# Performance work log

Hardware: AMD Instinct MI355X
Metric: run time of the kernel (lower is better)

## Reference

```python
import jax, jax.numpy as jnp
import numpy as np

S, B, I, H = 512, 8192, 3, 5  # seq, batch, input_size, hidden_size


def _uniform(key, shape, bound):
    return jax.random.uniform(key, shape, jnp.float32, -bound, bound)


def setup_inputs() -> dict:
    key = jax.random.key(0)
    ks = jax.random.split(key, 17)
    bound = 1.0 / np.sqrt(H)
    inp = {"x": jax.random.normal(ks[0], (S, B, I), jnp.float32)}
    # layer 0: in=I ; layer 1: in=2H (concat of both directions). Suffix 'r' = reverse direction.
    specs = [
        ("l0", I), ("l0r", I), ("l1", 2 * H), ("l1r", 2 * H),
    ]
    ki = 1
    for name, din in specs:
        inp[f"w_ih_{name}"] = _uniform(ks[ki], (4 * H, din), bound); ki += 1
        inp[f"w_hh_{name}"] = _uniform(ks[ki], (4 * H, H), bound); ki += 1
        inp[f"b_ih_{name}"] = _uniform(ks[ki], (4 * H,), bound); ki += 1
        inp[f"b_hh_{name}"] = _uniform(ks[ki], (4 * H,), bound); ki += 1
    return inp


def _lstm_dir(x, w_ih, w_hh, b_ih, b_hh, reverse):
    """Single-direction LSTM over x [S,B,Din] -> (hs [S,B,H], h_T [B,H], c_T [B,H])."""
    xs = x[::-1] if reverse else x
    # Precompute input contributions for all timesteps in one big matmul.
    gx = jnp.einsum('sbi,gi->sbg', xs, w_ih) + b_ih + b_hh  # [S,B,4H]
    h0 = jnp.zeros((x.shape[1], H), x.dtype)
    c0 = jnp.zeros((x.shape[1], H), x.dtype)

    def step(carry, g):
        h, c = carry
        g = g + h @ w_hh.T  # [B,4H]
        i, f, gg, o = jnp.split(g, 4, axis=-1)  # PyTorch gate order: i,f,g,o
        i = jax.nn.sigmoid(i)
        f = jax.nn.sigmoid(f)
        gg = jnp.tanh(gg)
        o = jax.nn.sigmoid(o)
        c = f * c + i * gg
        h = o * jnp.tanh(c)
        return (h, c), h

    (hT, cT), hs = jax.lax.scan(step, (h0, c0), gx)
    if reverse:
        hs = hs[::-1]
    return hs, hT, cT


def reference(x,
              w_ih_l0, w_hh_l0, b_ih_l0, b_hh_l0,
              w_ih_l0r, w_hh_l0r, b_ih_l0r, b_hh_l0r,
              w_ih_l1, w_hh_l1, b_ih_l1, b_hh_l1,
              w_ih_l1r, w_hh_l1r, b_ih_l1r, b_hh_l1r):
    # Layer 0 (bidirectional)
    hs0f, h0f, c0f = _lstm_dir(x, w_ih_l0, w_hh_l0, b_ih_l0, b_hh_l0, False)
    hs0b, h0b, c0b = _lstm_dir(x, w_ih_l0r, w_hh_l0r, b_ih_l0r, b_hh_l0r, True)
    out0 = jnp.concatenate([hs0f, hs0b], axis=-1)  # [S,B,2H]
    # Layer 1 (bidirectional) consumes concat of both directions
    hs1f, h1f, c1f = _lstm_dir(out0, w_ih_l1, w_hh_l1, b_ih_l1, b_hh_l1, False)
    hs1b, h1b, c1b = _lstm_dir(out0, w_ih_l1r, w_hh_l1r, b_ih_l1r, b_hh_l1r, True)
    output = jnp.concatenate([hs1f, hs1b], axis=-1)  # [S,B,2H]
    # PyTorch h_n/c_n layout: [num_layers*num_directions, B, H] ordered (l0 fwd, l0 bwd, l1 fwd, l1 bwd)
    h_n = jnp.stack([h0f, h0b, h1f, h1b], axis=0)
    c_n = jnp.stack([c0f, c0b, c1f, c1b], axis=0)
    return output, h_n, c_n
```

## Files before the change

kernel.cpp:

```cpp
#include <hip/hip_runtime.h>


constexpr int S_ = 512;
constexpr int B_ = 8192;
constexpr int NROW = 16384;

constexpr int GD1  = 2048;
constexpr int TL   = 240;
constexpr int GSTR = GD1 * 64;

constexpr float L2E  = 1.4426950408889634f;
constexpr float T2E  = 2.8853900817779268f;
constexpr float IT2E = 0.34657359027997264f;

typedef _Float16 v2h __attribute__((ext_vector_type(2)));

__device__ __forceinline__ float dot2h(v2h a, v2h b, float c) {
#if __has_builtin(__builtin_amdgcn_fdot2)
    return __builtin_amdgcn_fdot2(a, b, c, false);
#else
    return fmaf((float)a[0], (float)b[0], fmaf((float)a[1], (float)b[1], c));
#endif
}

__device__ __forceinline__ float rcp_(float x) { return __builtin_amdgcn_rcpf(x); }

__device__ __forceinline__ float exp2_(float x) {
#if __has_builtin(__builtin_amdgcn_exp2f)
    return __builtin_amdgcn_exp2f(x);
#else
    return exp2f(x);
#endif
}

__device__ __forceinline__ void sbar() { __builtin_amdgcn_sched_barrier(0); }

__device__ __forceinline__ float bperm(int bidx, float v) {
    return __int_as_float(__builtin_amdgcn_ds_bpermute(bidx, __float_as_int(v)));
}

__device__ __forceinline__ unsigned pkh(float a, float b) {
    auto t = __builtin_amdgcn_cvt_pkrtz(a, b);
    unsigned q; __builtin_memcpy(&q, &t, 4); return q;
}

__device__ __forceinline__ unsigned short f2h(float x) {
    _Float16 h = (_Float16)x;
    unsigned short s; __builtin_memcpy(&s, &h, 2); return s;
}

__device__ __forceinline__ float h2f(unsigned short s) {
    _Float16 h; __builtin_memcpy(&h, &s, 2); return (float)h;
}

__global__ __launch_bounds__(64) __attribute__((amdgpu_waves_per_eu(1, 2)))
void lstm_layer0(
    const float* __restrict__ x,
    const float* __restrict__ wih_f, const float* __restrict__ whh_f,
    const float* __restrict__ bih_f, const float* __restrict__ bhh_f,
    const float* __restrict__ wih_r, const float* __restrict__ whh_r,
    const float* __restrict__ bih_r, const float* __restrict__ bhh_r,
    unsigned short* __restrict__ ws,
    float* __restrict__ outbase)
{
    const int l64 = threadIdx.x & 63;
    int r = l64 / 5; r = (r > 11) ? 11 : r;
    const int u   = l64 - r * 5;
    const int uc  = (u < 5) ? u : 4;
    const int gid = blockIdx.x * 12 + r;
    const bool valid = gid < NROW;
    const int dir = (gid >> 13) & 1;
    const int b   = gid & 8191;
    const bool stw = valid && (u < 3);
    const bool st  = valid && (u < 5);

    int bidx[5];
#pragma unroll
    for (int k = 0; k < 5; k++) bidx[k] = (r * 5 + k) * 4;

    const float* __restrict__ wih = dir ? wih_r : wih_f;
    const float* __restrict__ whh = dir ? whh_r : whh_f;
    const float* __restrict__ bih = dir ? bih_r : bih_f;
    const float* __restrict__ bhh = dir ? bhh_r : bhh_f;

    const int rows[4] = {uc, 5 + uc, 10 + uc, 15 + uc};
    const float scl[4] = {-L2E, -L2E, T2E, -L2E};
    float WX[4][3], WH[4][5], BS[4];
#pragma unroll
    for (int gi = 0; gi < 4; gi++) {
        const int rr = rows[gi]; const float sc = scl[gi];
#pragma unroll
        for (int i = 0; i < 3; i++) WX[gi][i] = wih[rr * 3 + i] * sc;
#pragma unroll
        for (int k = 0; k < 5; k++) WH[gi][k] = whh[rr * 5 + k] * sc;
        BS[gi] = (bih[rr] + bhh[rr]) * sc;
    }

    float h[5] = {0.f, 0.f, 0.f, 0.f, 0.f};
    float cp = 0.f, hu_last = 0.f;

    const int t0 = dir ? (S_ - 1) : 0;
    const float* xp = x + ((size_t)t0 * B_ + b) * 3;
    unsigned short* wp = ws + (size_t)dir * ((size_t)S_ * B_ * 6)
                            + ((size_t)t0 * B_ + b) * 6;
    const ptrdiff_t xst = dir ? -(ptrdiff_t)3 * B_ : (ptrdiff_t)3 * B_;
    const ptrdiff_t wst = dir ? -(ptrdiff_t)6 * B_ : (ptrdiff_t)6 * B_;

    auto step = [&](const float (&xin)[3], unsigned short* wpp) {
        float a0 = BS[0], a1 = BS[1], a2 = BS[2], a3 = BS[3];
#pragma unroll
        for (int i = 0; i < 3; i++) {
            a0 = fmaf(WX[0][i], xin[i], a0);
            a1 = fmaf(WX[1][i], xin[i], a1);
            a2 = fmaf(WX[2][i], xin[i], a2);
            a3 = fmaf(WX[3][i], xin[i], a3);
        }
#pragma unroll
        for (int k = 0; k < 5; k++) {
            a0 = fmaf(WH[0][k], h[k], a0);
            a1 = fmaf(WH[1][k], h[k], a1);
            a2 = fmaf(WH[2][k], h[k], a2);
            a3 = fmaf(WH[3][k], h[k], a3);
        }
        const float ig = rcp_(1.0f + exp2_(a0));
        const float fg = rcp_(1.0f + exp2_(a1));
        const float g2 = fmaf(-2.0f * T2E, rcp_(1.0f + exp2_(a2)), T2E);
        const float og = rcp_(1.0f + exp2_(a3));
        cp = fmaf(fg, cp, ig * g2);
        const float th = fmaf(-2.0f, rcp_(1.0f + exp2_(cp)), 1.0f);
        const float hu = og * th;
        hu_last = hu;
#pragma unroll
        for (int k = 0; k < 5; k++) h[k] = bperm(bidx[k], hu);
        const unsigned q0 = pkh(h[0], h[1]);
        const unsigned q1 = pkh(h[2], h[3]);
        const unsigned q2 = pkh(h[4], 0.0f);
        unsigned qs = q0;
        qs = (u == 1) ? q1 : qs;
        qs = (u == 2) ? q2 : qs;
        if (stw) ((unsigned*)wpp)[u] = qs;
    };

    auto ld = [&](float (&buf)[3]) {
        __builtin_memcpy(&buf[0], xp, 12);
        xp += xst;
        sbar();
    };

    float x0[3], x1[3], x2[3], x3[3], x4[3], x5[3], x6[3], x7[3];
    ld(x0); ld(x1); ld(x2); ld(x3); ld(x4); ld(x5); ld(x6); ld(x7);

#pragma unroll 1
    for (int s = 0; s < S_ - 8; s += 8) {
        step(x0, wp); wp += wst; ld(x0);
        step(x1, wp); wp += wst; ld(x1);
        step(x2, wp); wp += wst; ld(x2);
        step(x3, wp); wp += wst; ld(x3);
        step(x4, wp); wp += wst; ld(x4);
        step(x5, wp); wp += wst; ld(x5);
        step(x6, wp); wp += wst; ld(x6);
        step(x7, wp); wp += wst; ld(x7);
    }
    step(x0, wp); wp += wst;
    step(x1, wp); wp += wst;
    step(x2, wp); wp += wst;
    step(x3, wp); wp += wst;
    step(x4, wp); wp += wst;
    step(x5, wp); wp += wst;
    step(x6, wp); wp += wst;
    step(x7, wp);

    const size_t OUTE = (size_t)S_ * B_ * 10;
    float* hn = outbase + OUTE + ((size_t)dir * B_ + b) * 5;
    float* cn = hn + (size_t)4 * B_ * 5;
    if (st) { hn[uc] = hu_last; cn[uc] = cp * IT2E; }
}

__global__ __launch_bounds__(64) __attribute__((amdgpu_waves_per_eu(2, 4)))
void lstm_layer1(
    const unsigned short* __restrict__ ws,
    const float* __restrict__ wih_f, const float* __restrict__ whh_f,
    const float* __restrict__ bih_f, const float* __restrict__ bhh_f,
    const float* __restrict__ wih_r, const float* __restrict__ whh_r,
    const float* __restrict__ bih_r, const float* __restrict__ bhh_r,
    float* __restrict__ outbase,
    unsigned short* __restrict__ gtemp)
{
    __shared__ unsigned short lt[TL * 40];

    const int l64 = threadIdx.x & 63;
    const int bid = (int)blockIdx.x;
    const int bsw = (bid & 7) * 256 + (bid >> 3);
    const int r  = l64 >> 3;
    const int u  = l64 & 7;
    const int uc = (u < 5) ? u : 4;
    const int rm  = r & 3;
    const int dir = r >> 2;
    const int b   = bsw * 4 + rm;
    const bool st = (u < 5);
    const int dir5 = dir * 5;
    const int pr  = dir ? (r - 4) : (r + 4);
    const int psL = pr * 5 + uc;
    const int psG = pr * 8 + uc;

    const float* __restrict__ wih = dir ? wih_r : wih_f;
    const float* __restrict__ whh = dir ? whh_r : whh_f;
    const float* __restrict__ bih = dir ? bih_r : bih_f;
    const float* __restrict__ bhh = dir ? bhh_r : bhh_f;

    const int rows[4] = {uc, 5 + uc, 10 + uc, 15 + uc};
    const float scl[4] = {-L2E, -L2E, T2E, -L2E};
    v2h WX[4][6];
    float WH[4][5], BS[4];
#pragma unroll
    for (int gi = 0; gi < 4; gi++) {
        const int rr = rows[gi]; const float sc = scl[gi];
#pragma unroll
        for (int p = 0; p < 6; p++) {
            const int i0 = (p < 3) ? 2 * p : 2 * p - 1;
            const bool pad = (p == 2) || (p == 5);
            const float w0 = wih[rr * 10 + i0] * sc;
            const float w1 = pad ? 0.f : wih[rr * 10 + i0 + 1] * sc;
            WX[gi][p] = (v2h){(_Float16)w0, (_Float16)w1};
        }
#pragma unroll
        for (int k = 0; k < 5; k++) WH[gi][k] = whh[rr * 5 + k] * sc;
        BS[gi] = (bih[rr] + bhh[rr]) * sc;
    }

    float h[5] = {0.f, 0.f, 0.f, 0.f, 0.f};
    float cp = 0.f, hu_last = 0.f;

    const int t0 = dir ? (S_ - 1) : 0;
    const unsigned short* rpf = ws + ((size_t)t0 * B_ + b) * 6;
    const unsigned short* rpb = rpf + (size_t)S_ * B_ * 6;
    float* op = outbase + ((size_t)(dir ? 255 : 256) * B_ + b) * 10;
    const ptrdiff_t rst = dir ? -(ptrdiff_t)6 * B_ : (ptrdiff_t)6 * B_;
    const ptrdiff_t ost = dir ? -(ptrdiff_t)10 * B_ : (ptrdiff_t)10 * B_;

    unsigned short* gw = gtemp + (size_t)bid * 64 + l64;

    struct A4 { float a0, a1, a2, a3; };

    auto dots = [&](const v2h (&xin)[6]) -> A4 {
        A4 v;
        v.a0 = BS[0]; v.a1 = BS[1]; v.a2 = BS[2]; v.a3 = BS[3];
#pragma unroll
        for (int p = 0; p < 6; p++) {
            v.a0 = dot2h(xin[p], WX[0][p], v.a0);
            v.a1 = dot2h(xin[p], WX[1][p], v.a1);
            v.a2 = dot2h(xin[p], WX[2][p], v.a2);
            v.a3 = dot2h(xin[p], WX[3][p], v.a3);
        }
        return v;
    };

    auto cell = [&](A4 v) -> float {
#pragma unroll
        for (int k = 0; k < 5; k++) {
            v.a0 = fmaf(WH[0][k], h[k], v.a0);
            v.a1 = fmaf(WH[1][k], h[k], v.a1);
            v.a2 = fmaf(WH[2][k], h[k], v.a2);
            v.a3 = fmaf(WH[3][k], h[k], v.a3);
        }
        const float ig = rcp_(1.0f + exp2_(v.a0));
        const float fg = rcp_(1.0f + exp2_(v.a1));
        const float g2 = fmaf(-2.0f * T2E, rcp_(1.0f + exp2_(v.a2)), T2E);
        const float og = rcp_(1.0f + exp2_(v.a3));
        cp = fmaf(fg, cp, ig * g2);
        const float th = fmaf(-2.0f, rcp_(1.0f + exp2_(cp)), 1.0f);
        const float hu = og * th;
        hu_last = hu;
        return hu;
    };

    auto bcast = [&](float hu) {
        const int v = __float_as_int(hu);
        h[0] = __int_as_float(__builtin_amdgcn_ds_swizzle(v, 0x18 | (0 << 5)));
        h[1] = __int_as_float(__builtin_amdgcn_ds_swizzle(v, 0x18 | (1 << 5)));
        h[2] = __int_as_float(__builtin_amdgcn_ds_swizzle(v, 0x18 | (2 << 5)));
        h[3] = __int_as_float(__builtin_amdgcn_ds_swizzle(v, 0x18 | (3 << 5)));
        h[4] = __int_as_float(__builtin_amdgcn_ds_swizzle(v, 0x18 | (4 << 5)));
    };

    auto ld = [&](v2h (&buf)[6]) {
        __builtin_memcpy(&buf[0], rpf, 12);
        __builtin_memcpy(&buf[3], rpb, 12);
        rpf += rst; rpb += rst;
        sbar();
    };

    auto s1L = [&](v2h (&xb)[6], int t) {
        A4 a = dots(xb); ld(xb);
        const float hu = cell(a); bcast(hu);
        if (st) lt[t * 40 + r * 5 + u] = f2h(hu);
    };
    auto s1G = [&](v2h (&xb)[6]) {
        A4 a = dots(xb); ld(xb);
        const float hu = cell(a); bcast(hu);
        *gw = f2h(hu); gw += GSTR;
    };
    auto s2G = [&](v2h (&xb)[6], unsigned short pvs) {
        A4 a = dots(xb); ld(xb);
        const float pv = h2f(pvs);
        const float hu = cell(a); bcast(hu);
        if (st) { op[dir5 + u] = hu; op[5 - dir5 + u] = pv; }
        op += ost;
    };
    auto s2L = [&](v2h (&xb)[6], int t) {
        const float pv = h2f(lt[(511 - t) * 40 + psL]);
        A4 a = dots(xb); ld(xb);
        const float hu = cell(a); bcast(hu);
        if (st) { op[dir5 + u] = hu; op[5 - dir5 + u] = pv; }
        op += ost;
    };
    auto s2Ln = [&](v2h (&xb)[6], int t) {
        const float pv = h2f(lt[(511 - t) * 40 + psL]);
        A4 a = dots(xb);
        const float hu = cell(a); bcast(hu);
        if (st) { op[dir5 + u] = hu; op[5 - dir5 + u] = pv; }
        op += ost;
    };

    v2h x0[6], x1[6], x2[6], x3[6], x4[6], x5[6], x6[6], x7[6];
    ld(x0); ld(x1); ld(x2); ld(x3); ld(x4); ld(x5); ld(x6); ld(x7);

#pragma unroll 1
    for (int t = 0; t < TL; t += 8) {
        s1L(x0, t + 0); s1L(x1, t + 1); s1L(x2, t + 2); s1L(x3, t + 3);
        s1L(x4, t + 4); s1L(x5, t + 5); s1L(x6, t + 6); s1L(x7, t + 7);
    }
#pragma unroll 1
    for (int t = TL; t < 256; t += 8) {
        s1G(x0); s1G(x1); s1G(x2); s1G(x3);
        s1G(x4); s1G(x5); s1G(x6); s1G(x7);
    }
    asm volatile("s_waitcnt vmcnt(0)" ::: "memory");
    const unsigned short* g0 = gtemp + (size_t)bid * 64 + psG;
    const unsigned short q15 = g0[(size_t)15 * GSTR];
    const unsigned short q14 = g0[(size_t)14 * GSTR];
    const unsigned short q13 = g0[(size_t)13 * GSTR];
    const unsigned short q12 = g0[(size_t)12 * GSTR];
    const unsigned short q11 = g0[(size_t)11 * GSTR];
    const unsigned short q10 = g0[(size_t)10 * GSTR];
    const unsigned short q9  = g0[(size_t)9  * GSTR];
    const unsigned short q8  = g0[(size_t)8  * GSTR];
    const unsigned short q7  = g0[(size_t)7  * GSTR];
    const unsigned short q6  = g0[(size_t)6  * GSTR];
    const unsigned short q5  = g0[(size_t)5  * GSTR];
    const unsigned short q4  = g0[(size_t)4  * GSTR];
    const unsigned short q3  = g0[(size_t)3  * GSTR];
    const unsigned short q2  = g0[(size_t)2  * GSTR];
    const unsigned short q1  = g0[(size_t)1  * GSTR];
    const unsigned short q0  = g0[0];
    s2G(x0, q15); s2G(x1, q14); s2G(x2, q13); s2G(x3, q12);
    s2G(x4, q11); s2G(x5, q10); s2G(x6, q9);  s2G(x7, q8);
    s2G(x0, q7);  s2G(x1, q6);  s2G(x2, q5);  s2G(x3, q4);
    s2G(x4, q3);  s2G(x5, q2);  s2G(x6, q1);  s2G(x7, q0);
#pragma unroll 1
    for (int t = 272; t < 504; t += 8) {
        s2L(x0, t + 0); s2L(x1, t + 1); s2L(x2, t + 2); s2L(x3, t + 3);
        s2L(x4, t + 4); s2L(x5, t + 5); s2L(x6, t + 6); s2L(x7, t + 7);
    }
    s2Ln(x0, 504); s2Ln(x1, 505); s2Ln(x2, 506); s2Ln(x3, 507);
    s2Ln(x4, 508); s2Ln(x5, 509); s2Ln(x6, 510); s2Ln(x7, 511);

    const size_t OUTE = (size_t)S_ * B_ * 10;
    float* hn = outbase + OUTE + ((size_t)(2 + dir) * B_ + b) * 5;
    float* cn = hn + (size_t)4 * B_ * 5;
    if (st) { hn[u] = hu_last; cn[u] = cp * IT2E; }
}

extern "C" void kernel_launch(void* const* d_in, const int* in_sizes, int n_in,
                              void* d_out, int out_size, void* d_ws, size_t ws_size,
                              hipStream_t stream) {
    const float* x       = (const float*)d_in[0];
    const float* wih_l0  = (const float*)d_in[1];
    const float* whh_l0  = (const float*)d_in[2];
    const float* bih_l0  = (const float*)d_in[3];
    const float* bhh_l0  = (const float*)d_in[4];
    const float* wih_l0r = (const float*)d_in[5];
    const float* whh_l0r = (const float*)d_in[6];
    const float* bih_l0r = (const float*)d_in[7];
    const float* bhh_l0r = (const float*)d_in[8];
    const float* wih_l1  = (const float*)d_in[9];
    const float* whh_l1  = (const float*)d_in[10];
    const float* bih_l1  = (const float*)d_in[11];
    const float* bhh_l1  = (const float*)d_in[12];
    const float* wih_l1r = (const float*)d_in[13];
    const float* whh_l1r = (const float*)d_in[14];
    const float* bih_l1r = (const float*)d_in[15];
    const float* bhh_l1r = (const float*)d_in[16];

    float* out = (float*)d_out;
    unsigned short* ws = (unsigned short*)d_ws;
    unsigned short* gtemp = ws + (size_t)2 * S_ * B_ * 6;

    dim3 grid0(1366), block(64);
    lstm_layer0<<<grid0, block, 0, stream>>>(x,
        wih_l0, whh_l0, bih_l0, bhh_l0,
        wih_l0r, whh_l0r, bih_l0r, bhh_l0r,
        ws, out);
    dim3 grid1(GD1);
    lstm_layer1<<<grid1, block, 0, stream>>>(ws,
        wih_l1, whh_l1, bih_l1, bhh_l1,
        wih_l1r, whh_l1r, bih_l1r, bhh_l1r,
        out, gtemp);
}
```

Before: 308.9 us.

## Pack 12 rows per wave in layer1 with XCD-aware block swizzle

Layer 1 now maps 12 sequence rows per 64-lane wave (5 lanes each, 6 batches × 2 directions) instead of 8 rows with 8 lanes, reducing the grid from 2048 to 1366 blocks. The hidden-state broadcast switches from ds_swizzle to ds_bpermute to fit the 5-lane groups. The LDS history buffer and global spill split are retuned (TL 208, a 48-step global region read through a rolling 4-deep prefetch). Both kernels use an XCD-aware block index remap. Fewer idle lanes per wave means less total work, at the cost of bpermute latency on the serial recurrence and more global spill traffic.

Measured after the change: 310.7 us. Within noise of the previous version (+0.6%).

```diff
diff --git a/kernel.cpp b/kernel.cpp
--- a/kernel.cpp
+++ b/kernel.cpp
@@ -5,8 +5,8 @@
 constexpr int B_ = 8192;
 constexpr int NROW = 16384;
 
-constexpr int GD1  = 2048;
-constexpr int TL   = 240;
+constexpr int GD1  = 1366;
+constexpr int TL   = 208;
 constexpr int GSTR = GD1 * 64;
 
 constexpr float L2E  = 1.4426950408889634f;
@@ -51,6 +51,12 @@
 
 __device__ __forceinline__ float h2f(unsigned short s) {
     _Float16 h; __builtin_memcpy(&h, &s, 2); return (float)h;
+}
+
+__device__ __forceinline__ int xswz1366(int bid) {
+    const int xcd = bid & 7, loc = bid >> 3;
+    const int base = (xcd < 6) ? xcd * 171 : 1026 + (xcd - 6) * 170;
+    return base + loc;
 }
 
 __global__ __launch_bounds__(64) __attribute__((amdgpu_waves_per_eu(1, 2)))
@@ -67,7 +73,8 @@
     int r = l64 / 5; r = (r > 11) ? 11 : r;
     const int u   = l64 - r * 5;
     const int uc  = (u < 5) ? u : 4;
-    const int gid = blockIdx.x * 12 + r;
+    const int bsw = xswz1366((int)blockIdx.x);
+    const int gid = bsw * 12 + r;
     const bool valid = gid < NROW;
     const int dir = (gid >> 13) & 1;
     const int b   = gid & 8191;
@@ -176,7 +183,7 @@
     if (st) { hn[uc] = hu_last; cn[uc] = cp * IT2E; }
 }
 
-__global__ __launch_bounds__(64) __attribute__((amdgpu_waves_per_eu(2, 4)))
+__global__ __launch_bounds__(64) __attribute__((amdgpu_waves_per_eu(1, 2)))
 void lstm_layer1(
     const unsigned short* __restrict__ ws,
     const float* __restrict__ wih_f, const float* __restrict__ whh_f,
@@ -186,22 +193,28 @@
     float* __restrict__ outbase,
     unsigned short* __restrict__ gtemp)
 {
-    __shared__ unsigned short lt[TL * 40];
+    __shared__ unsigned short lt[TL * 60];
 
     const int l64 = threadIdx.x & 63;
     const int bid = (int)blockIdx.x;
-    const int bsw = (bid & 7) * 256 + (bid >> 3);
-    const int r  = l64 >> 3;
-    const int u  = l64 & 7;
-    const int uc = (u < 5) ? u : 4;
-    const int rm  = r & 3;
-    const int dir = r >> 2;
-    const int b   = bsw * 4 + rm;
-    const bool st = (u < 5);
+    const int bsw = xswz1366(bid);
+    int r = l64 / 5; r = (r > 11) ? 11 : r;
+    const int u   = l64 - r * 5;
+    const int uc  = (u < 5) ? u : 4;
+    const int rm  = (r < 6) ? r : r - 6;
+    const int dir = (r >= 6) ? 1 : 0;
+    const int braw = bsw * 6 + rm;
+    const bool valid = braw < B_;
+    const int b   = valid ? braw : (B_ - 1);
+    const bool st = valid && (u < 5);
+    const bool lw = (l64 < 60);
     const int dir5 = dir * 5;
-    const int pr  = dir ? (r - 4) : (r + 4);
-    const int psL = pr * 5 + uc;
-    const int psG = pr * 8 + uc;
+    const int pr  = dir ? (r - 6) : (r + 6);
+    const int ps  = pr * 5 + uc;
+
+    int bidx[5];
+#pragma unroll
+    for (int k = 0; k < 5; k++) bidx[k] = (r * 5 + k) * 4;
 
     const float* __restrict__ wih = dir ? wih_r : wih_f;
     const float* __restrict__ whh = dir ? whh_r : whh_f;
@@ -275,12 +288,8 @@
     };
 
     auto bcast = [&](float hu) {
-        const int v = __float_as_int(hu);
-        h[0] = __int_as_float(__builtin_amdgcn_ds_swizzle(v, 0x18 | (0 << 5)));
-        h[1] = __int_as_float(__builtin_amdgcn_ds_swizzle(v, 0x18 | (1 << 5)));
-        h[2] = __int_as_float(__builtin_amdgcn_ds_swizzle(v, 0x18 | (2 << 5)));
-        h[3] = __int_as_float(__builtin_amdgcn_ds_swizzle(v, 0x18 | (3 << 5)));
-        h[4] = __int_as_float(__builtin_amdgcn_ds_swizzle(v, 0x18 | (4 << 5)));
+#pragma unroll
+        for (int k = 0; k < 5; k++) h[k] = bperm(bidx[k], hu);
     };
 
     auto ld = [&](v2h (&buf)[6]) {
@@ -293,7 +302,7 @@
     auto s1L = [&](v2h (&xb)[6], int t) {
         A4 a = dots(xb); ld(xb);
         const float hu = cell(a); bcast(hu);
-        if (st) lt[t * 40 + r * 5 + u] = f2h(hu);
+        if (lw) lt[t * 60 + l64] = f2h(hu);
     };
     auto s1G = [&](v2h (&xb)[6]) {
         A4 a = dots(xb); ld(xb);
@@ -304,21 +313,21 @@
         A4 a = dots(xb); ld(xb);
         const float pv = h2f(pvs);
         const float hu = cell(a); bcast(hu);
-        if (st) { op[dir5 + u] = hu; op[5 - dir5 + u] = pv; }
+        if (st) { op[dir5 + uc] = hu; op[5 - dir5 + uc] = pv; }
         op += ost;
     };
     auto s2L = [&](v2h (&xb)[6], int t) {
-        const float pv = h2f(lt[(511 - t) * 40 + psL]);
+        const float pv = h2f(lt[(511 - t) * 60 + ps]);
         A4 a = dots(xb); ld(xb);
         const float hu = cell(a); bcast(hu);
-        if (st) { op[dir5 + u] = hu; op[5 - dir5 + u] = pv; }
+        if (st) { op[dir5 + uc] = hu; op[5 - dir5 + uc] = pv; }
         op += ost;
     };
     auto s2Ln = [&](v2h (&xb)[6], int t) {
-        const float pv = h2f(lt[(511 - t) * 40 + psL]);
+        const float pv = h2f(lt[(511 - t) * 60 + ps]);
         A4 a = dots(xb);
         const float hu = cell(a); bcast(hu);
-        if (st) { op[dir5 + u] = hu; op[5 - dir5 + u] = pv; }
+        if (st) { op[dir5 + uc] = hu; op[5 - dir5 + uc] = pv; }
         op += ost;
     };
 
@@ -336,29 +345,25 @@
         s1G(x4); s1G(x5); s1G(x6); s1G(x7);
     }
     asm volatile("s_waitcnt vmcnt(0)" ::: "memory");
-    const unsigned short* g0 = gtemp + (size_t)bid * 64 + psG;
-    const unsigned short q15 = g0[(size_t)15 * GSTR];
-    const unsigned short q14 = g0[(size_t)14 * GSTR];
-    const unsigned short q13 = g0[(size_t)13 * GSTR];
-    const unsigned short q12 = g0[(size_t)12 * GSTR];
-    const unsigned short q11 = g0[(size_t)11 * GSTR];
-    const unsigned short q10 = g0[(size_t)10 * GSTR];
-    const unsigned short q9  = g0[(size_t)9  * GSTR];
-    const unsigned short q8  = g0[(size_t)8  * GSTR];
-    const unsigned short q7  = g0[(size_t)7  * GSTR];
-    const unsigned short q6  = g0[(size_t)6  * GSTR];
-    const unsigned short q5  = g0[(size_t)5  * GSTR];
-    const unsigned short q4  = g0[(size_t)4  * GSTR];
-    const unsigned short q3  = g0[(size_t)3  * GSTR];
-    const unsigned short q2  = g0[(size_t)2  * GSTR];
-    const unsigned short q1  = g0[(size_t)1  * GSTR];
-    const unsigned short q0  = g0[0];
-    s2G(x0, q15); s2G(x1, q14); s2G(x2, q13); s2G(x3, q12);
-    s2G(x4, q11); s2G(x5, q10); s2G(x6, q9);  s2G(x7, q8);
-    s2G(x0, q7);  s2G(x1, q6);  s2G(x2, q5);  s2G(x3, q4);
-    s2G(x4, q3);  s2G(x5, q2);  s2G(x6, q1);  s2G(x7, q0);
+    const unsigned short* gb = gtemp + (size_t)bid * 64 + ps;
+    unsigned short q0 = gb[(size_t)47 * GSTR];
+    unsigned short q1 = gb[(size_t)46 * GSTR];
+    unsigned short q2 = gb[(size_t)45 * GSTR];
+    unsigned short q3 = gb[(size_t)44 * GSTR];
+    const unsigned short* grq = gb + (size_t)43 * GSTR;
 #pragma unroll 1
-    for (int t = 272; t < 504; t += 8) {
+    for (int t = 256; t < 304; t += 8) {
+        s2G(x0, q0); q0 = *grq; grq -= GSTR;
+        s2G(x1, q1); q1 = *grq; grq -= GSTR;
+        s2G(x2, q2); q2 = *grq; grq -= GSTR;
+        s2G(x3, q3); q3 = *grq; grq -= GSTR;
+        s2G(x4, q0); q0 = *grq; grq -= GSTR;
+        s2G(x5, q1); q1 = *grq; grq -= GSTR;
+        s2G(x6, q2); q2 = *grq; grq -= GSTR;
+        s2G(x7, q3); q3 = *grq; grq -= GSTR;
+    }
+#pragma unroll 1
+    for (int t = 304; t < 504; t += 8) {
         s2L(x0, t + 0); s2L(x1, t + 1); s2L(x2, t + 2); s2L(x3, t + 3);
         s2L(x4, t + 4); s2L(x5, t + 5); s2L(x6, t + 6); s2L(x7, t + 7);
     }
@@ -368,7 +373,7 @@
     const size_t OUTE = (size_t)S_ * B_ * 10;
     float* hn = outbase + OUTE + ((size_t)(2 + dir) * B_ + b) * 5;
     float* cn = hn + (size_t)4 * B_ * 5;
-    if (st) { hn[u] = hu_last; cn[u] = cp * IT2E; }
+    if (st) { hn[uc] = hu_last; cn[uc] = cp * IT2E; }
 }
 
 extern "C" void kernel_launch(void* const* d_in, const int* in_sizes, int n_in,
@@ -394,7 +399,7 @@
 
     float* out = (float*)d_out;
     unsigned short* ws = (unsigned short*)d_ws;
-    unsigned short* gtemp = ws + (size_t)2 * S_ * B_ * 6;
+    unsigned short* gtemp = ws + (size_t)2 * S_ * B_ * 6 + (size_t)4 * GSTR;
 
     dim3 grid0(1366), block(64);
     lstm_layer0<<<grid0, block, 0, stream>>>(x,
```
